# Performance work log

Hardware: AMD Instinct MI355X
Metric: run time of the kernel (lower is better)

Reference implementation:

```python
import jax, jax.numpy as jnp
import numpy as np

HEAD_DIM = 64  # init arg `dim`; scale divisor is sqrt(dim)


def setup_inputs() -> dict:
    key = jax.random.key(0)
    k1, k2 = jax.random.split(key)
    x1 = jax.random.normal(k1, (16, 2048, 64), dtype=jnp.float32)
    x2 = jax.random.normal(k2, (16, 2048, 64), dtype=jnp.float32)
    return {"x1": x1, "x2": x2}


def reference(x1, x2):
    # qk: [B, Sq, Sk]
    qk = jnp.einsum("bqd,bkd->bqk", x1, x2)
    inv_scale = jnp.sqrt(jnp.asarray(HEAD_DIM, dtype=x1.dtype))
    attn = jax.nn.softmax(qk / inv_scale, axis=-1)
    # dropout is identity in eval / p=0
    out = jnp.einsum("bqk,bkd->bqd", attn, x2)
    return out
```

## Files before the change

### kernel.cpp

```cpp
#include <hip/hip_runtime.h>
#include <hip/hip_bf16.h>


typedef __attribute__((ext_vector_type(8))) short short8;
typedef __attribute__((ext_vector_type(16))) float f32x16;

#define MFMA32(a, b, c) __builtin_amdgcn_mfma_f32_32x32x16_bf16(a, b, c, 0, 0, 0)

union frag_u { short8 s8; unsigned u[4]; };

static __device__ __forceinline__ unsigned pk2(float a, float b) {
    __hip_bfloat162 h = __float22bfloat162_rn(float2{a, b});
    union { __hip_bfloat162 h2; unsigned u; } cv;
    cv.h2 = h;
    return cv.u;
}

static __device__ __forceinline__ short8 cvt8(const float* p, float sc) {
    float4 a = *(const float4*)p;
    float4 b = *(const float4*)(p + 4);
    frag_u f;
    f.u[0] = pk2(a.x * sc, a.y * sc);
    f.u[1] = pk2(a.z * sc, a.w * sc);
    f.u[2] = pk2(b.x * sc, b.y * sc);
    f.u[3] = pk2(b.z * sc, b.w * sc);
    return f.s8;
}

static __device__ __forceinline__ void pl32swap(unsigned& a, unsigned& b) {
    asm("v_permlane32_swap_b32 %0, %1" : "+v"(a), "+v"(b));
}

__global__ __launch_bounds__(256) void prep_kernel(
    const float* __restrict__ x2, short* __restrict__ kf, short* __restrict__ vf)
{
    int idx = blockIdx.x * 256 + threadIdx.x;
    int chunk = idx >> 6;
    int l = idx & 63;
    int lo = l & 31, hi = l >> 5;
    int c = chunk & 4095;
    int b = c >> 8;
    int kt = (c >> 2) & 63;
    if (chunk < 4096) {
        int ds = c & 3;
        const float* src = x2 + ((size_t)(b * 2048 + kt * 32 + lo)) * 64 + ds * 16 + 8 * hi;
        ((short8*)kf)[(size_t)c * 64 + l] = cvt8(src, 1.0f);
    } else {
        int ks = (c >> 1) & 1;
        int dc = c & 1;
        const float* base = x2 + ((size_t)(b * 2048 + kt * 32 + ks * 16 + 8 * hi)) * 64 + dc * 32 + lo;
        frag_u o;
#pragma unroll
        for (int jj = 0; jj < 4; ++jj)
            o.u[jj] = pk2(base[(2 * jj) * 64], base[(2 * jj + 1) * 64]);
        ((short8*)vf)[(size_t)c * 64 + l] = o.s8;
    }
}

__global__ __launch_bounds__(256) void attn_kernel(
    const float* __restrict__ x1,
    const short* __restrict__ kf, const short* __restrict__ vf,
    float* __restrict__ out)
{
    __shared__ float ldo[4][32][64];
    __shared__ float ldl[4][64];

    const int l  = threadIdx.x & 63;
    const int w  = threadIdx.x >> 6;
    const int lo = l & 31, hi = l >> 5;

    const int bid = blockIdx.x;
    const int wi  = bid >> 3;
    const int b   = (bid & 7) * 2 + (wi >> 6);
    const int qt  = wi & 63;
    const int qrow = qt * 32 + lo;
    const size_t bbase = (size_t)b * 2048 * 64;

    const float QSC = 0.125f * 1.4426950408889634f;
    short8 qf[4];
    const float* qp = x1 + bbase + (size_t)qrow * 64 + 8 * hi;
#pragma unroll
    for (int ds = 0; ds < 4; ++ds) qf[ds] = cvt8(qp + ds * 16, QSC);

    f32x16 oacc0, oacc1;
#pragma unroll
    for (int r = 0; r < 16; ++r) { oacc0[r] = 0.f; oacc1[r] = 0.f; }
    float lsum = 0.f;

    const short8* kc = (const short8*)kf + (size_t)((b * 64 + w * 16) * 4) * 64 + l;
    const short8* vc = (const short8*)vf + (size_t)((b * 64 + w * 16) * 4) * 64 + l;

    for (int kt = 0; kt < 16; ++kt, kc += 256, vc += 256) {
        short8 k0 = kc[0], k1 = kc[64], k2 = kc[128], k3 = kc[192];
        f32x16 s;
#pragma unroll
        for (int r = 0; r < 16; ++r) s[r] = 0.f;
        s = MFMA32(k0, qf[0], s);
        s = MFMA32(k1, qf[1], s);
        s = MFMA32(k2, qf[2], s);
        s = MFMA32(k3, qf[3], s);

        float p[16];
        float rs = 0.f;
#pragma unroll
        for (int r = 0; r < 16; ++r) { p[r] = __builtin_amdgcn_exp2f(s[r]); rs += p[r]; }
        lsum += rs;

        unsigned pw[8];
#pragma unroll
        for (int i = 0; i < 8; ++i) pw[i] = pk2(p[2 * i], p[2 * i + 1]);
        pl32swap(pw[0], pw[2]);
        pl32swap(pw[1], pw[3]);
        pl32swap(pw[4], pw[6]);
        pl32swap(pw[5], pw[7]);
        frag_u pb0, pb1;
        pb0.u[0] = pw[0]; pb0.u[1] = pw[1]; pb0.u[2] = pw[2]; pb0.u[3] = pw[3];
        pb1.u[0] = pw[4]; pb1.u[1] = pw[5]; pb1.u[2] = pw[6]; pb1.u[3] = pw[7];

        short8 v00 = vc[0], v01 = vc[64], v10 = vc[128], v11 = vc[192];
        oacc0 = MFMA32(v00, pb0.s8, oacc0);
        oacc1 = MFMA32(v01, pb0.s8, oacc1);
        oacc0 = MFMA32(v10, pb1.s8, oacc0);
        oacc1 = MFMA32(v11, pb1.s8, oacc1);
    }

    float* myo = &ldo[w][0][0] + l;
#pragma unroll
    for (int r = 0; r < 16; ++r) {
        myo[r * 64]        = oacc0[r];
        myo[(16 + r) * 64] = oacc1[r];
    }
    ldl[w][l] = lsum;
    __syncthreads();

    float lt = 0.f;
#pragma unroll
    for (int ww = 0; ww < 4; ++ww) lt += ldl[ww][lo] + ldl[ww][lo + 32];
    float inv = 1.0f / lt;

    float* op = out + bbase + (size_t)qrow * 64;
#pragma unroll
    for (int i = 0; i < 8; ++i) {
        int rr = w * 8 + i;
        float v = ldo[0][rr][l] + ldo[1][rr][l] + ldo[2][rr][l] + ldo[3][rr][l];
        int r = rr & 15;
        int d = (r & 3) + 8 * (r >> 2) + 4 * hi + 32 * (rr >> 4);
        op[d] = v * inv;
    }
}

extern "C" void kernel_launch(void* const* d_in, const int* in_sizes, int n_in,
                              void* d_out, int out_size, void* d_ws, size_t ws_size,
                              hipStream_t stream) {
    const float* x1 = (const float*)d_in[0];
    const float* x2 = (const float*)d_in[1];
    float* out = (float*)d_out;

    short* kf = (short*)d_ws;
    short* vf = kf + (size_t)4096 * 512;

    hipLaunchKernelGGL(prep_kernel, dim3(2048), dim3(256), 0, stream, x2, kf, vf);
    hipLaunchKernelGGL(attn_kernel, dim3(1024), dim3(256), 0, stream, x1, kf, vf, out);
}
```

Measured before the change: 42.11 us.

## Share K/V tiles across two query-tile waves via double-buffered LDS

Restructures the attention kernel so each 128-thread block handles two query tiles, one per wave, with each wave iterating over all 64 key tiles. K/V fragments are loaded cooperatively into double-buffered shared memory and reused by both waves, replacing the split-K across four waves and the cross-wave LDS reduction at the end. It also adds s_setprio around MFMA groups and an inline v_cvt_pk_bf16_f32 conversion. The trade-off is a longer serial loop per wave, a block-wide barrier every iteration, and half as many blocks (512 instead of 1024), which lowers available parallelism.

```diff
diff --git a/kernel.cpp b/kernel.cpp
--- a/kernel.cpp
+++ b/kernel.cpp
@@ -14,6 +14,12 @@
     union { __hip_bfloat162 h2; unsigned u; } cv;
     cv.h2 = h;
     return cv.u;
+}
+
+static __device__ __forceinline__ unsigned cvtpk(float a, float b) {
+    unsigned r;
+    asm("v_cvt_pk_bf16_f32 %0, %1, %2" : "=v"(r) : "v"(a), "v"(b));
+    return r;
 }
 
 static __device__ __forceinline__ short8 cvt8(const float* p, float sc) {
@@ -57,13 +63,13 @@
     }
 }
 
-__global__ __launch_bounds__(256) void attn_kernel(
+__global__ __launch_bounds__(128) void attn_kernel(
     const float* __restrict__ x1,
     const short* __restrict__ kf, const short* __restrict__ vf,
     float* __restrict__ out)
 {
-    __shared__ float ldo[4][32][64];
-    __shared__ float ldl[4][64];
+    __shared__ short8 kbuf[2][4][64];
+    __shared__ short8 vbuf[2][4][64];
 
     const int l  = threadIdx.x & 63;
     const int w  = threadIdx.x >> 6;
@@ -71,8 +77,9 @@
 
     const int bid = blockIdx.x;
     const int wi  = bid >> 3;
-    const int b   = (bid & 7) * 2 + (wi >> 6);
-    const int qt  = wi & 63;
+    const int b   = (bid & 7) * 2 + (wi >> 5);
+    const int qb  = wi & 31;
+    const int qt  = qb * 2 + w;
     const int qrow = qt * 32 + lo;
     const size_t bbase = (size_t)b * 2048 * 64;
 
@@ -87,28 +94,50 @@
     for (int r = 0; r < 16; ++r) { oacc0[r] = 0.f; oacc1[r] = 0.f; }
     float lsum = 0.f;
 
-    const short8* kc = (const short8*)kf + (size_t)((b * 64 + w * 16) * 4) * 64 + l;
-    const short8* vc = (const short8*)vf + (size_t)((b * 64 + w * 16) * 4) * 64 + l;
+    const short8* kg = (const short8*)kf + (size_t)(b * 64) * 256;
+    const short8* vg = (const short8*)vf + (size_t)(b * 64) * 256;
 
-    for (int kt = 0; kt < 16; ++kt, kc += 256, vc += 256) {
-        short8 k0 = kc[0], k1 = kc[64], k2 = kc[128], k3 = kc[192];
+    const int c0 = 2 * w, c1 = c0 + 1;
+
+    short8 ks0 = kg[c0 * 64 + l], ks1 = kg[c1 * 64 + l];
+    short8 vs0 = vg[c0 * 64 + l], vs1 = vg[c1 * 64 + l];
+    kbuf[0][c0][l] = ks0; kbuf[0][c1][l] = ks1;
+    vbuf[0][c0][l] = vs0; vbuf[0][c1][l] = vs1;
+    __syncthreads();
+
+#pragma unroll 2
+    for (int kt = 0; kt < 64; ++kt) {
+        const int cur = kt & 1, nxt = cur ^ 1;
+
+        if (kt < 63) {
+            const size_t nb = (size_t)(kt + 1) * 256;
+            ks0 = kg[nb + c0 * 64 + l]; ks1 = kg[nb + c1 * 64 + l];
+            vs0 = vg[nb + c0 * 64 + l]; vs1 = vg[nb + c1 * 64 + l];
+        }
+
+        short8 k0 = kbuf[cur][0][l], k1 = kbuf[cur][1][l],
+               k2 = kbuf[cur][2][l], k3 = kbuf[cur][3][l];
         f32x16 s;
 #pragma unroll
         for (int r = 0; r < 16; ++r) s[r] = 0.f;
+        __builtin_amdgcn_s_setprio(1);
         s = MFMA32(k0, qf[0], s);
         s = MFMA32(k1, qf[1], s);
         s = MFMA32(k2, qf[2], s);
         s = MFMA32(k3, qf[3], s);
+        __builtin_amdgcn_s_setprio(0);
 
-        float p[16];
+        unsigned pw[8];
         float rs = 0.f;
 #pragma unroll
-        for (int r = 0; r < 16; ++r) { p[r] = __builtin_amdgcn_exp2f(s[r]); rs += p[r]; }
+        for (int i = 0; i < 8; ++i) {
+            float pa = __builtin_amdgcn_exp2f(s[2 * i]);
+            float pb = __builtin_amdgcn_exp2f(s[2 * i + 1]);
+            rs += pa + pb;
+            pw[i] = cvtpk(pa, pb);
+        }
         lsum += rs;
 
-        unsigned pw[8];
-#pragma unroll
-        for (int i = 0; i < 8; ++i) pw[i] = pk2(p[2 * i], p[2 * i + 1]);
         pl32swap(pw[0], pw[2]);
         pl32swap(pw[1], pw[3]);
         pl32swap(pw[4], pw[6]);
@@ -117,35 +146,30 @@
         pb0.u[0] = pw[0]; pb0.u[1] = pw[1]; pb0.u[2] = pw[2]; pb0.u[3] = pw[3];
         pb1.u[0] = pw[4]; pb1.u[1] = pw[5]; pb1.u[2] = pw[6]; pb1.u[3] = pw[7];
 
-        short8 v00 = vc[0], v01 = vc[64], v10 = vc[128], v11 = vc[192];
-        oacc0 = MFMA32(v00, pb0.s8, oacc0);
-        oacc1 = MFMA32(v01, pb0.s8, oacc1);
-        oacc0 = MFMA32(v10, pb1.s8, oacc0);
-        oacc1 = MFMA32(v11, pb1.s8, oacc1);
+        short8 v0 = vbuf[cur][0][l], v1 = vbuf[cur][1][l],
+               v2 = vbuf[cur][2][l], v3 = vbuf[cur][3][l];
+        __builtin_amdgcn_s_setprio(1);
+        oacc0 = MFMA32(v0, pb0.s8, oacc0);
+        oacc1 = MFMA32(v1, pb0.s8, oacc1);
+        oacc0 = MFMA32(v2, pb1.s8, oacc0);
+        oacc1 = MFMA32(v3, pb1.s8, oacc1);
+        __builtin_amdgcn_s_setprio(0);
+
+        if (kt < 63) {
+            kbuf[nxt][c0][l] = ks0; kbuf[nxt][c1][l] = ks1;
+            vbuf[nxt][c0][l] = vs0; vbuf[nxt][c1][l] = vs1;
+        }
+        __syncthreads();
     }
 
-    float* myo = &ldo[w][0][0] + l;
+    float lt = lsum + __shfl_xor(lsum, 32);
+    float inv = 1.0f / lt;
+    float* op = out + bbase + (size_t)qrow * 64;
 #pragma unroll
     for (int r = 0; r < 16; ++r) {
-        myo[r * 64]        = oacc0[r];
-        myo[(16 + r) * 64] = oacc1[r];
-    }
-    ldl[w][l] = lsum;
-    __syncthreads();
-
-    float lt = 0.f;
-#pragma unroll
-    for (int ww = 0; ww < 4; ++ww) lt += ldl[ww][lo] + ldl[ww][lo + 32];
-    float inv = 1.0f / lt;
-
-    float* op = out + bbase + (size_t)qrow * 64;
-#pragma unroll
-    for (int i = 0; i < 8; ++i) {
-        int rr = w * 8 + i;
-        float v = ldo[0][rr][l] + ldo[1][rr][l] + ldo[2][rr][l] + ldo[3][rr][l];
-        int r = rr & 15;
-        int d = (r & 3) + 8 * (r >> 2) + 4 * hi + 32 * (rr >> 4);
-        op[d] = v * inv;
+        int d = (r & 3) + 8 * (r >> 2) + 4 * hi;
+        op[d]      = oacc0[r] * inv;
+        op[32 + d] = oacc1[r] * inv;
     }
 }
 
@@ -160,5 +184,5 @@
     short* vf = kf + (size_t)4096 * 512;
 
     hipLaunchKernelGGL(prep_kernel, dim3(2048), dim3(256), 0, stream, x2, kf, vf);
-    hipLaunchKernelGGL(attn_kernel, dim3(1024), dim3(256), 0, stream, x1, kf, vf, out);
+    hipLaunchKernelGGL(attn_kernel, dim3(512), dim3(128), 0, stream, x1, kf, vf, out);
 }
```

Result: slower. 53.25 us (+26.4%).
